# Kernel optimization log

Hardware: AMD Instinct MI355X
Metric: run time of the kernel (lower is better)

The kernel has to match this reference:

```python
import jax, jax.numpy as jnp
import numpy as np

B, T, C = 2, 2048, 1024
H = 4 * C           # MLP hidden (4*n_embd)
E_DYN = 7           # num_experts - static_experts
TOP_K = 2           # num_experts_per_tok
MOE_LOSS_COEF = 0.01


def setup_inputs() -> dict:
    key = jax.random.key(0)
    ks = jax.random.split(key, 6)
    s = 0.02
    x = jax.random.normal(ks[0], (B, T, C), dtype=jnp.float32)
    gate_w = jax.random.normal(ks[1], (C, E_DYN), dtype=jnp.float32) * s
    w1 = jax.random.normal(ks[2], (E_DYN, C, H), dtype=jnp.float32) * s   # dynamic experts c_fc
    w2 = jax.random.normal(ks[3], (E_DYN, H, C), dtype=jnp.float32) * s   # dynamic experts c_proj
    w1s = jax.random.normal(ks[4], (C, H), dtype=jnp.float32) * s         # static expert c_fc
    w2s = jax.random.normal(ks[5], (H, C), dtype=jnp.float32) * s         # static expert c_proj
    return {"x": x, "gate_w": gate_w, "w1": w1, "w2": w2, "w1s": w1s, "w2s": w2s}


def reference(x, gate_w, w1, w2, w1s, w2s):
    b, t, c = x.shape
    xf = x.reshape(-1, c)                                   # [N, C]
    n = xf.shape[0]

    # static expert (always applied)
    y_static = jax.nn.gelu(xf @ w1s, approximate=False) @ w2s  # [N, C]

    # gating: top-k + softmax over selected scores
    scores = xf @ gate_w                                    # [N, E]
    topk_scores, topk_idx = jax.lax.top_k(scores, TOP_K)    # [N, K]
    topk_w = jax.nn.softmax(topk_scores, axis=-1)           # [N, K]

    # dense dispatch weights [N, E] (top_k indices are distinct -> set is safe)
    probs = jnp.zeros((n, E_DYN), dtype=x.dtype)
    probs = probs.at[jnp.arange(n)[:, None], topk_idx].set(topk_w)

    # all-expert MLP then weighted combine (same math as masked per-expert dispatch)
    h = jax.nn.gelu(jnp.einsum('nc,ech->enh', xf, w1), approximate=False)  # [E, N, H]
    y_all = jnp.einsum('enh,ehc->enc', h, w2)               # [E, N, C]
    y_dyn = jnp.einsum('ne,enc->nc', probs, y_all)          # [N, C]

    y = (y_dyn + y_static).reshape(b, t, c)

    # variance_penalty auxiliary loss
    expert_usage = probs.mean(axis=0)                       # [E]
    variance = jnp.mean((expert_usage - expert_usage.mean()) ** 2)
    aux = MOE_LOSS_COEF * variance
    return y, aux
```

## Files before the change

### kernel.cpp

```cpp
#include <hip/hip_runtime.h>
#include <hip/hip_bf16.h>
#include <math.h>

#define N_TOK 4096
#define C_DIM 1024
#define H_DIM 4096
#define NEXP 7
#define NGRP 8
#define HCAP 13184

typedef __attribute__((ext_vector_type(8))) short short8;
typedef __attribute__((ext_vector_type(4))) float floatx4;

static const size_t OFF_COUNTS = 0;
static const size_t OFF_CURSOR = 64;
static const size_t OFF_BASE   = 128;
static const size_t OFF_PCOUNT = 192;
static const size_t OFF_CNT8   = 256;
static const size_t OFF_USAGE  = 320;
static const size_t OFF_TOPKI  = 4096;
static const size_t OFF_TOPKW  = OFF_TOPKI + 8192ull * 4;
static const size_t OFF_ETOK   = OFF_TOPKW + 8192ull * 4;
static const size_t OFF_EWT    = OFF_ETOK + (size_t)HCAP * 4;
static const size_t OFF_EIDX   = OFF_EWT + (size_t)HCAP * 4;
static const size_t OFF_XB     = 262144;
static const size_t OFF_W1T    = OFF_XB + (size_t)N_TOK * C_DIM * 2;
static const size_t OFF_W2T    = OFF_W1T + (size_t)NGRP * H_DIM * C_DIM * 2;
static const size_t OFF_H      = OFF_W2T + (size_t)NGRP * C_DIM * H_DIM * 2;

static __device__ __forceinline__ unsigned short f2bf(float f) {
    __hip_bfloat16 b = __float2bfloat16(f);
    return *reinterpret_cast<unsigned short*>(&b);
}
static __device__ __forceinline__ float bf2f(unsigned short u) {
    unsigned int v = ((unsigned int)u) << 16;
    return __builtin_bit_cast(float, v);
}

static __device__ __forceinline__ float gelu_f(float v) {
    float z = v * 0.70710678118654752f;
    float az = fabsf(z);
    float t = 1.0f / (1.0f + 0.3275911f * az);
    float poly = t * (0.254829592f + t * (-0.284496736f + t * (1.421413741f +
                 t * (-1.453152027f + t * 1.061405429f))));
    float erf_abs = 1.0f - poly * __expf(-az * az);
    float erf_v = (z < 0.f) ? -erf_abs : erf_abs;
    return 0.5f * v * (1.0f + erf_v);
}

static __device__ __forceinline__ void gll16(const void* g, void* l) {
    __builtin_amdgcn_global_load_lds((const __attribute__((address_space(1))) void*)g,
                                     (__attribute__((address_space(3))) void*)l, 16, 0, 0);
}

__global__ void init_small_kernel(int* counts, int* cursor, float* usage) {
    int i = threadIdx.x;
    if (i < 8) { counts[i] = 0; cursor[i] = 0; usage[i] = 0.f; }
}

__global__ void convert_x_kernel(const float* __restrict__ x, unsigned short* __restrict__ xb) {
    int i = blockIdx.x * 256 + threadIdx.x;
    float4 v = ((const float4*)x)[i];
    ushort4 o;
    o.x = f2bf(v.x); o.y = f2bf(v.y); o.z = f2bf(v.z); o.w = f2bf(v.w);
    ((ushort4*)xb)[i] = o;
}

__global__ __launch_bounds__(256) void transpose_cvt_kernel(
    const float* __restrict__ dyn, const float* __restrict__ stat,
    __hip_bfloat16* __restrict__ dst, int R, int S)
{
    int e = blockIdx.z;
    const float* src = (e < NEXP) ? (dyn + (size_t)e * R * S) : stat;
    __hip_bfloat16* d = dst + (size_t)e * R * S;
    int s0 = blockIdx.x * 32, r0 = blockIdx.y * 64;
    int tx = threadIdx.x & 31, ty = threadIdx.x >> 5;
    __shared__ float t[64][33];
#pragma unroll
    for (int i = 0; i < 8; i++) {
        int r = ty + i * 8;
        t[r][tx] = src[(size_t)(r0 + r) * S + s0 + tx];
    }
    __syncthreads();
    int tx2 = threadIdx.x & 63, ty2 = threadIdx.x >> 6;
#pragma unroll
    for (int i = 0; i < 8; i++) {
        int s = ty2 + i * 4;
        d[(size_t)(s0 + s) * R + r0 + tx2] = __float2bfloat16(t[tx2][s]);
    }
}

__global__ __launch_bounds__(256) void gate_kernel(
    const float* __restrict__ x, const float* __restrict__ gw,
    int* __restrict__ topki, float* __restrict__ topkw,
    int* counts, float* usage)
{
    int wid = threadIdx.x >> 6, lane = threadIdx.x & 63;
    int t = blockIdx.x * 4 + wid;
    float s[NEXP];
#pragma unroll
    for (int e = 0; e < NEXP; e++) s[e] = 0.f;
    for (int c = lane; c < C_DIM; c += 64) {
        float xv = x[(size_t)t * C_DIM + c];
#pragma unroll
        for (int e = 0; e < NEXP; e++) s[e] += xv * gw[c * NEXP + e];
    }
#pragma unroll
    for (int e = 0; e < NEXP; e++)
        for (int off = 32; off > 0; off >>= 1) s[e] += __shfl_xor(s[e], off);
    if (lane == 0) {
        int e0 = 0;
        for (int e = 1; e < NEXP; e++) if (s[e] > s[e0]) e0 = e;
        int e1 = -1;
        for (int e = 0; e < NEXP; e++) {
            if (e == e0) continue;
            if (e1 < 0 || s[e] > s[e1]) e1 = e;
        }
        float w0 = 1.f / (1.f + expf(s[e1] - s[e0]));
        float w1 = 1.f - w0;
        topki[t * 2] = e0; topki[t * 2 + 1] = e1;
        topkw[t * 2] = w0; topkw[t * 2 + 1] = w1;
        atomicAdd(&counts[e0], 1); atomicAdd(&counts[e1], 1);
        atomicAdd(&usage[e0], w0); atomicAdd(&usage[e1], w1);
    }
}

__global__ __launch_bounds__(256) void prefix_kernel(
    const int* counts, const float* usage,
    int* base, int* pcount, int* cnt8,
    int* etok, float* ewt, float* y, int aux_index)
{
    __shared__ int sb[NGRP], sc[NGRP], sp[NGRP];
    if (threadIdx.x == 0) {
        int run = 0;
        for (int g = 0; g < NEXP; g++) {
            int c = counts[g];
            int p = (c + 127) & ~127;
            base[g] = run; pcount[g] = p; cnt8[g] = c;
            sb[g] = run; sc[g] = c; sp[g] = p;
            run += p;
        }
        base[NEXP] = run; pcount[NEXP] = N_TOK; cnt8[NEXP] = N_TOK;
        sb[NEXP] = run; sc[NEXP] = N_TOK; sp[NEXP] = N_TOK;
        float u[NEXP]; float mean = 0.f;
        for (int e = 0; e < NEXP; e++) { u[e] = usage[e] / (float)N_TOK; mean += u[e]; }
        mean /= (float)NEXP;
        float var = 0.f;
        for (int e = 0; e < NEXP; e++) { float d = u[e] - mean; var += d * d; }
        var /= (float)NEXP;
        y[aux_index] = 0.01f * var;
    }
    __syncthreads();
    for (int i = threadIdx.x; i < N_TOK; i += 256) {
        etok[sb[NEXP] + i] = i; ewt[sb[NEXP] + i] = 1.0f;
    }
    for (int g = 0; g < NEXP; g++) {
        for (int i = sc[g] + (int)threadIdx.x; i < sp[g]; i += 256) {
            etok[sb[g] + i] = 0; ewt[sb[g] + i] = 0.f;
        }
    }
}

__global__ void scatter_kernel(const int* __restrict__ topki, const float* __restrict__ topkw,
                               const int* __restrict__ base, int* cursor,
                               int* __restrict__ etok, float* __restrict__ ewt,
                               int* __restrict__ eidx)
{
    int i = blockIdx.x * 256 + threadIdx.x;
    int t = i >> 1;
    int e = topki[i];
    float w = topkw[i];
    int pos = atomicAdd(&cursor[e], 1);
    int idx = base[e] + pos;
    etok[idx] = t; ewt[idx] = w;
    eidx[i] = idx;
}

__global__ __launch_bounds__(256) void gemm1_kernel(
    const __hip_bfloat16* __restrict__ xb,
    const __hip_bfloat16* __restrict__ w1t,
    __hip_bfloat16* __restrict__ h,
    const int* __restrict__ etok,
    const int* __restrict__ base,
    const int* __restrict__ pcount)
{
    int g = blockIdx.z, mt = blockIdx.y, ct = blockIdx.x;
    if (mt * 128 >= pcount[g]) return;
    int eb = base[g];

    __shared__ __align__(16) char AlsB[2 * 8192];
    __shared__ __align__(16) char BlsB[2 * 8192];

    int tid = threadIdx.x;
    int lane = tid & 63, wid = tid >> 6;
    int quad = lane >> 4, l16 = lane & 15;
    int wm = wid >> 1, wn = wid & 1;
    int rsub = lane >> 2, chunk = lane & 3;

    const char* gA[2]; const char* gB[2];
    char* lA[2]; char* lB[2];
#pragma unroll
    for (int j = 0; j < 2; j++) {
        int rowA = wid * 32 + j * 16 + rsub;
        int tok = etok[eb + mt * 128 + rowA];
        gA[j] = (const char*)(xb + (size_t)tok * C_DIM) + chunk * 16;
        lA[j] = AlsB + (wid * 32 + j * 16) * 64;
        int rowB = wid * 32 + j * 16 + rsub;
        gB[j] = (const char*)(w1t + ((size_t)g * H_DIM + ct * 128 + rowB) * C_DIM) + chunk * 16;
        lB[j] = BlsB + (wid * 32 + j * 16) * 64;
    }

    floatx4 acc[4][4] = {};
    for (int k0 = 0; k0 < C_DIM; k0 += 64) {
        size_t koff = (size_t)k0 * 2;
#pragma unroll
        for (int s = 0; s < 2; s++) {
            size_t so = koff + (size_t)s * 64;
            gll16(gA[0] + so, lA[0] + s * 8192);
            gll16(gA[1] + so, lA[1] + s * 8192);
            gll16(gB[0] + so, lB[0] + s * 8192);
            gll16(gB[1] + so, lB[1] + s * 8192);
        }
        __syncthreads();
#pragma unroll
        for (int s = 0; s < 2; s++) {
            short8 a[4], b[4];
#pragma unroll
            for (int i = 0; i < 4; i++) {
                a[i] = *(const short8*)(AlsB + s * 8192 + (((wm * 64 + i * 16 + l16) * 32 + quad * 8) * 2));
                b[i] = *(const short8*)(BlsB + s * 8192 + (((wn * 64 + i * 16 + l16) * 32 + quad * 8) * 2));
            }
#pragma unroll
            for (int i = 0; i < 4; i++)
#pragma unroll
                for (int j = 0; j < 4; j++)
                    acc[i][j] = __builtin_amdgcn_mfma_f32_16x16x32_bf16(a[i], b[j], acc[i][j], 0, 0, 0);
        }
        __syncthreads();
    }

#pragma unroll
    for (int i = 0; i < 4; i++) {
        int rbase = mt * 128 + wm * 64 + i * 16 + quad * 4;
#pragma unroll
        for (int reg = 0; reg < 4; reg++) {
            size_t hrow = (size_t)(eb + rbase + reg) * H_DIM;
#pragma unroll
            for (int j = 0; j < 4; j++) {
                int cc = ct * 128 + wn * 64 + j * 16 + l16;
                h[hrow + cc] = __float2bfloat16(gelu_f(acc[i][j][reg]));
            }
        }
    }
}

__global__ __launch_bounds__(256) void gemm2_kernel(
    const __hip_bfloat16* __restrict__ h,
    const __hip_bfloat16* __restrict__ w2t,
    unsigned short* __restrict__ yp,
    const int* __restrict__ base,
    const int* __restrict__ pcount)
{
    int g = blockIdx.z, ct = blockIdx.x, mt = blockIdx.y;
    if (mt * 128 >= pcount[g]) return;
    int eb = base[g];

    __shared__ __align__(16) char AlsB[2 * 8192];
    __shared__ __align__(16) char BlsB[2 * 8192];

    int tid = threadIdx.x;
    int lane = tid & 63, wid = tid >> 6;
    int quad = lane >> 4, l16 = lane & 15;
    int wm = wid >> 1, wn = wid & 1;
    int rsub = lane >> 2, chunk = lane & 3;

    const char* gA[2]; const char* gB[2];
    char* lA[2]; char* lB[2];
#pragma unroll
    for (int j = 0; j < 2; j++) {
        int rowA = wid * 32 + j * 16 + rsub;
        gA[j] = (const char*)(h + (size_t)(eb + mt * 128 + rowA) * H_DIM) + chunk * 16;
        lA[j] = AlsB + (wid * 32 + j * 16) * 64;
        int rowB = wid * 32 + j * 16 + rsub;
        gB[j] = (const char*)(w2t + ((size_t)g * C_DIM + ct * 128 + rowB) * H_DIM) + chunk * 16;
        lB[j] = BlsB + (wid * 32 + j * 16) * 64;
    }

    floatx4 acc[4][4] = {};
    for (int k0 = 0; k0 < H_DIM; k0 += 64) {
        size_t koff = (size_t)k0 * 2;
#pragma unroll
        for (int s = 0; s < 2; s++) {
            size_t so = koff + (size_t)s * 64;
            gll16(gA[0] + so, lA[0] + s * 8192);
            gll16(gA[1] + so, lA[1] + s * 8192);
            gll16(gB[0] + so, lB[0] + s * 8192);
            gll16(gB[1] + so, lB[1] + s * 8192);
        }
        __syncthreads();
#pragma unroll
        for (int s = 0; s < 2; s++) {
            short8 a[4], b[4];
#pragma unroll
            for (int i = 0; i < 4; i++) {
                a[i] = *(const short8*)(AlsB + s * 8192 + (((wm * 64 + i * 16 + l16) * 32 + quad * 8) * 2));
                b[i] = *(const short8*)(BlsB + s * 8192 + (((wn * 64 + i * 16 + l16) * 32 + quad * 8) * 2));
            }
#pragma unroll
            for (int i = 0; i < 4; i++)
#pragma unroll
                for (int j = 0; j < 4; j++)
                    acc[i][j] = __builtin_amdgcn_mfma_f32_16x16x32_bf16(a[i], b[j], acc[i][j], 0, 0, 0);
        }
        __syncthreads();
    }

#pragma unroll
    for (int i = 0; i < 4; i++) {
        int rl0 = mt * 128 + wm * 64 + i * 16 + quad * 4;
#pragma unroll
        for (int reg = 0; reg < 4; reg++) {
            size_t yrow = (size_t)(eb + rl0 + reg) * C_DIM;
#pragma unroll
            for (int j = 0; j < 4; j++) {
                int cc = ct * 128 + wn * 64 + j * 16 + l16;
                yp[yrow + cc] = f2bf(acc[i][j][reg]);
            }
        }
    }
}

__global__ __launch_bounds__(256) void combine_kernel(
    const unsigned short* __restrict__ yp,
    const int* __restrict__ eidx,
    const float* __restrict__ topkw,
    const int* __restrict__ base,
    float* __restrict__ y)
{
    int t = blockIdx.x;
    int i0 = eidx[t * 2], i1 = eidx[t * 2 + 1];
    float w0 = topkw[t * 2], w1 = topkw[t * 2 + 1];
    int is = base[NEXP] + t;
    int c = threadIdx.x * 4;
    ushort4 a = *(const ushort4*)(yp + (size_t)i0 * C_DIM + c);
    ushort4 b = *(const ushort4*)(yp + (size_t)i1 * C_DIM + c);
    ushort4 s = *(const ushort4*)(yp + (size_t)is * C_DIM + c);
    float4 o;
    o.x = w0 * bf2f(a.x) + w1 * bf2f(b.x) + bf2f(s.x);
    o.y = w0 * bf2f(a.y) + w1 * bf2f(b.y) + bf2f(s.y);
    o.z = w0 * bf2f(a.z) + w1 * bf2f(b.z) + bf2f(s.z);
    o.w = w0 * bf2f(a.w) + w1 * bf2f(b.w) + bf2f(s.w);
    *(float4*)(y + (size_t)t * C_DIM + c) = o;
}

extern "C" void kernel_launch(void* const* d_in, const int* in_sizes, int n_in,
                              void* d_out, int out_size, void* d_ws, size_t ws_size,
                              hipStream_t stream) {
    const float* x      = (const float*)d_in[0];
    const float* gate_w = (const float*)d_in[1];
    const float* w1     = (const float*)d_in[2];
    const float* w2     = (const float*)d_in[3];
    const float* w1s    = (const float*)d_in[4];
    const float* w2s    = (const float*)d_in[5];
    float* y = (float*)d_out;
    char* ws = (char*)d_ws;

    int*   counts = (int*)(ws + OFF_COUNTS);
    int*   cursor = (int*)(ws + OFF_CURSOR);
    int*   base   = (int*)(ws + OFF_BASE);
    int*   pcount = (int*)(ws + OFF_PCOUNT);
    int*   cnt8   = (int*)(ws + OFF_CNT8);
    float* usage  = (float*)(ws + OFF_USAGE);
    int*   topki  = (int*)(ws + OFF_TOPKI);
    float* topkw  = (float*)(ws + OFF_TOPKW);
    int*   etok   = (int*)(ws + OFF_ETOK);
    float* ewt    = (float*)(ws + OFF_EWT);
    int*   eidx   = (int*)(ws + OFF_EIDX);
    unsigned short* xb_u = (unsigned short*)(ws + OFF_XB);
    __hip_bfloat16* xb  = (__hip_bfloat16*)(ws + OFF_XB);
    __hip_bfloat16* w1t = (__hip_bfloat16*)(ws + OFF_W1T);
    __hip_bfloat16* w2t = (__hip_bfloat16*)(ws + OFF_W2T);
    __hip_bfloat16* hbuf = (__hip_bfloat16*)(ws + OFF_H);
    unsigned short* yp  = (unsigned short*)(ws + OFF_W1T);

    init_small_kernel<<<1, 64, 0, stream>>>(counts, cursor, usage);

    convert_x_kernel<<<(N_TOK * C_DIM / 4) / 256, 256, 0, stream>>>(x, xb_u);
    transpose_cvt_kernel<<<dim3(H_DIM / 32, C_DIM / 64, NGRP), 256, 0, stream>>>(w1, w1s, w1t, C_DIM, H_DIM);
    transpose_cvt_kernel<<<dim3(C_DIM / 32, H_DIM / 64, NGRP), 256, 0, stream>>>(w2, w2s, w2t, H_DIM, C_DIM);

    gate_kernel<<<N_TOK / 4, 256, 0, stream>>>(x, gate_w, topki, topkw, counts, usage);
    prefix_kernel<<<1, 256, 0, stream>>>(counts, usage, base, pcount, cnt8, etok, ewt, y, N_TOK * C_DIM);
    scatter_kernel<<<(N_TOK * 2) / 256, 256, 0, stream>>>(topki, topkw, base, cursor, etok, ewt, eidx);

    gemm1_kernel<<<dim3(H_DIM / 128, 64, NGRP), 256, 0, stream>>>(xb, w1t, hbuf, etok, base, pcount);
    gemm2_kernel<<<dim3(C_DIM / 128, 64, NGRP), 256, 0, stream>>>(hbuf, w2t, yp, base, pcount);
    combine_kernel<<<N_TOK, 256, 0, stream>>>(yp, eidx, topkw, base, y);
}
```

Baseline: 814.6 us.

## Triple-buffer GEMM K-loop with async loads, LDS swizzle, XCD-aware gemm2 tiling

Both expert GEMMs drop the two-sync-per-64K loop for a three-stage ring of 32-wide K tiles. Global-to-LDS loads are issued two stages ahead and waited on with explicit vmcnt and barrier calls, and the MFMA block is wrapped in setprio. LDS rows use an XOR chunk swizzle to cut bank conflicts. gemm2 moves to a 1D grid that keeps blocks sharing an mt tile on the same XCD for L2 reuse, and the weight transpose kernel now uses paired float2/ushort2 accesses. The hand-placed waitcnt and barrier sequence is fragile, and the third buffer adds LDS use, which may lower occupancy.

New measurement: 843.6 us. 1.04x slower.

```diff
diff --git a/kernel.cpp b/kernel.cpp
--- a/kernel.cpp
+++ b/kernel.cpp
@@ -53,6 +53,39 @@
                                      (__attribute__((address_space(3))) void*)l, 16, 0, 0);
 }
 
+template <int VM> static __device__ __forceinline__ void wait_vm() {
+    if constexpr (VM == 8) asm volatile("s_waitcnt vmcnt(8)" ::: "memory");
+    else if constexpr (VM == 4) asm volatile("s_waitcnt vmcnt(4)" ::: "memory");
+    else asm volatile("s_waitcnt vmcnt(0)" ::: "memory");
+}
+static __device__ __forceinline__ void barf() {
+    __builtin_amdgcn_s_barrier();
+    asm volatile("" ::: "memory");
+}
+static __device__ __forceinline__ void lgkm0_bar() {
+    asm volatile("s_waitcnt lgkmcnt(0)" ::: "memory");
+    __builtin_amdgcn_s_barrier();
+    asm volatile("" ::: "memory");
+}
+
+static __device__ __forceinline__ void mfma_step(const char* Ap, const char* Bp,
+    int wm, int wn, int l16, int rswz, floatx4 (&acc)[4][4])
+{
+    short8 a[4], b[4];
+#pragma unroll
+    for (int i = 0; i < 4; i++) {
+        a[i] = *(const short8*)(Ap + ((wm * 64 + i * 16 + l16) * 64 + rswz));
+        b[i] = *(const short8*)(Bp + ((wn * 64 + i * 16 + l16) * 64 + rswz));
+    }
+    __builtin_amdgcn_s_setprio(1);
+#pragma unroll
+    for (int i = 0; i < 4; i++)
+#pragma unroll
+        for (int j = 0; j < 4; j++)
+            acc[i][j] = __builtin_amdgcn_mfma_f32_16x16x32_bf16(a[i], b[j], acc[i][j], 0, 0, 0);
+    __builtin_amdgcn_s_setprio(0);
+}
+
 __global__ void init_small_kernel(int* counts, int* cursor, float* usage) {
     int i = threadIdx.x;
     if (i < 8) { counts[i] = 0; cursor[i] = 0; usage[i] = 0.f; }
@@ -72,21 +105,25 @@
 {
     int e = blockIdx.z;
     const float* src = (e < NEXP) ? (dyn + (size_t)e * R * S) : stat;
-    __hip_bfloat16* d = dst + (size_t)e * R * S;
+    unsigned short* d = (unsigned short*)(dst + (size_t)e * R * S);
     int s0 = blockIdx.x * 32, r0 = blockIdx.y * 64;
-    int tx = threadIdx.x & 31, ty = threadIdx.x >> 5;
     __shared__ float t[64][33];
-#pragma unroll
-    for (int i = 0; i < 8; i++) {
-        int r = ty + i * 8;
-        t[r][tx] = src[(size_t)(r0 + r) * S + s0 + tx];
+    int tx4 = threadIdx.x & 15, ty4 = threadIdx.x >> 4;
+#pragma unroll
+    for (int i = 0; i < 4; i++) {
+        int r = ty4 + i * 16;
+        float2 v = *(const float2*)(src + (size_t)(r0 + r) * S + s0 + tx4 * 2);
+        t[r][tx4 * 2] = v.x; t[r][tx4 * 2 + 1] = v.y;
     }
     __syncthreads();
-    int tx2 = threadIdx.x & 63, ty2 = threadIdx.x >> 6;
-#pragma unroll
-    for (int i = 0; i < 8; i++) {
-        int s = ty2 + i * 4;
-        d[(size_t)(s0 + s) * R + r0 + tx2] = __float2bfloat16(t[tx2][s]);
+    int tx3 = threadIdx.x & 31, ty3 = threadIdx.x >> 5;
+#pragma unroll
+    for (int i = 0; i < 4; i++) {
+        int s = ty3 + i * 8;
+        int r = tx3 * 2;
+        ushort2 o;
+        o.x = f2bf(t[r][s]); o.y = f2bf(t[r + 1][s]);
+        *(ushort2*)(d + (size_t)(s0 + s) * R + r0 + r) = o;
     }
 }
 
@@ -146,7 +183,7 @@
         for (int e = 0; e < NEXP; e++) { u[e] = usage[e] / (float)N_TOK; mean += u[e]; }
         mean /= (float)NEXP;
         float var = 0.f;
-        for (int e = 0; e < NEXP; e++) { float d = u[e] - mean; var += d * d; }
+        for (int e = 0; e < NEXP; e++) { float dd = u[e] - mean; var += dd * dd; }
         var /= (float)NEXP;
         y[aux_index] = 0.01f * var;
     }
@@ -188,56 +225,52 @@
     if (mt * 128 >= pcount[g]) return;
     int eb = base[g];
 
-    __shared__ __align__(16) char AlsB[2 * 8192];
-    __shared__ __align__(16) char BlsB[2 * 8192];
+    __shared__ __align__(16) char Ab[3][8192];
+    __shared__ __align__(16) char Bb[3][8192];
 
     int tid = threadIdx.x;
     int lane = tid & 63, wid = tid >> 6;
     int quad = lane >> 4, l16 = lane & 15;
     int wm = wid >> 1, wn = wid & 1;
     int rsub = lane >> 2, chunk = lane & 3;
-
-    const char* gA[2]; const char* gB[2];
-    char* lA[2]; char* lB[2];
+    int swzc = chunk ^ ((rsub >> 1) & 3);
+    int rswz = (quad ^ ((l16 >> 1) & 3)) * 16;
+
+    const char* gA[2]; const char* gB[2]; int lo[2];
 #pragma unroll
     for (int j = 0; j < 2; j++) {
-        int rowA = wid * 32 + j * 16 + rsub;
-        int tok = etok[eb + mt * 128 + rowA];
-        gA[j] = (const char*)(xb + (size_t)tok * C_DIM) + chunk * 16;
-        lA[j] = AlsB + (wid * 32 + j * 16) * 64;
-        int rowB = wid * 32 + j * 16 + rsub;
-        gB[j] = (const char*)(w1t + ((size_t)g * H_DIM + ct * 128 + rowB) * C_DIM) + chunk * 16;
-        lB[j] = BlsB + (wid * 32 + j * 16) * 64;
-    }
+        int row = wid * 32 + j * 16 + rsub;
+        int tok = etok[eb + mt * 128 + row];
+        gA[j] = (const char*)(xb + (size_t)tok * C_DIM) + swzc * 16;
+        gB[j] = (const char*)(w1t + ((size_t)g * H_DIM + ct * 128 + row) * C_DIM) + swzc * 16;
+        lo[j] = (wid * 32 + j * 16) * 64;
+    }
+
+#define STG(p, kt) do { size_t so = (size_t)(kt) * 64; \
+        gll16(gA[0] + so, Ab[p] + lo[0]); \
+        gll16(gA[1] + so, Ab[p] + lo[1]); \
+        gll16(gB[0] + so, Bb[p] + lo[0]); \
+        gll16(gB[1] + so, Bb[p] + lo[1]); } while (0)
 
     floatx4 acc[4][4] = {};
-    for (int k0 = 0; k0 < C_DIM; k0 += 64) {
-        size_t koff = (size_t)k0 * 2;
-#pragma unroll
-        for (int s = 0; s < 2; s++) {
-            size_t so = koff + (size_t)s * 64;
-            gll16(gA[0] + so, lA[0] + s * 8192);
-            gll16(gA[1] + so, lA[1] + s * 8192);
-            gll16(gB[0] + so, lB[0] + s * 8192);
-            gll16(gB[1] + so, lB[1] + s * 8192);
-        }
-        __syncthreads();
-#pragma unroll
-        for (int s = 0; s < 2; s++) {
-            short8 a[4], b[4];
-#pragma unroll
-            for (int i = 0; i < 4; i++) {
-                a[i] = *(const short8*)(AlsB + s * 8192 + (((wm * 64 + i * 16 + l16) * 32 + quad * 8) * 2));
-                b[i] = *(const short8*)(BlsB + s * 8192 + (((wn * 64 + i * 16 + l16) * 32 + quad * 8) * 2));
-            }
-#pragma unroll
-            for (int i = 0; i < 4; i++)
-#pragma unroll
-                for (int j = 0; j < 4; j++)
-                    acc[i][j] = __builtin_amdgcn_mfma_f32_16x16x32_bf16(a[i], b[j], acc[i][j], 0, 0, 0);
-        }
-        __syncthreads();
-    }
+    const int nt = C_DIM / 32;
+    STG(0, 0); STG(1, 1);
+    int p = 0;
+    for (int t = 0; t + 2 < nt; ++t) {
+        int pn = p + 2; if (pn >= 3) pn -= 3;
+        STG(pn, t + 2);
+        wait_vm<8>();
+        barf();
+        mfma_step(Ab[p], Bb[p], wm, wn, l16, rswz, acc);
+        lgkm0_bar();
+        if (++p == 3) p = 0;
+    }
+    wait_vm<4>(); barf();
+    mfma_step(Ab[0], Bb[0], wm, wn, l16, rswz, acc);
+    lgkm0_bar();
+    wait_vm<0>(); barf();
+    mfma_step(Ab[1], Bb[1], wm, wn, l16, rswz, acc);
+#undef STG
 
 #pragma unroll
     for (int i = 0; i < 4; i++) {
@@ -261,59 +294,60 @@
     const int* __restrict__ base,
     const int* __restrict__ pcount)
 {
-    int g = blockIdx.z, ct = blockIdx.x, mt = blockIdx.y;
+    int id = blockIdx.x;
+    int xcd = id & 7;
+    int jj  = id >> 3;
+    int ct  = jj & 7;
+    int g4  = xcd + ((jj >> 3) << 3);
+    int mt  = g4 & 63, g = g4 >> 6;
     if (mt * 128 >= pcount[g]) return;
     int eb = base[g];
 
-    __shared__ __align__(16) char AlsB[2 * 8192];
-    __shared__ __align__(16) char BlsB[2 * 8192];
+    __shared__ __align__(16) char Ab[3][8192];
+    __shared__ __align__(16) char Bb[3][8192];
 
     int tid = threadIdx.x;
     int lane = tid & 63, wid = tid >> 6;
     int quad = lane >> 4, l16 = lane & 15;
     int wm = wid >> 1, wn = wid & 1;
     int rsub = lane >> 2, chunk = lane & 3;
-
-    const char* gA[2]; const char* gB[2];
-    char* lA[2]; char* lB[2];
+    int swzc = chunk ^ ((rsub >> 1) & 3);
+    int rswz = (quad ^ ((l16 >> 1) & 3)) * 16;
+
+    const char* gA[2]; const char* gB[2]; int lo[2];
 #pragma unroll
     for (int j = 0; j < 2; j++) {
-        int rowA = wid * 32 + j * 16 + rsub;
-        gA[j] = (const char*)(h + (size_t)(eb + mt * 128 + rowA) * H_DIM) + chunk * 16;
-        lA[j] = AlsB + (wid * 32 + j * 16) * 64;
-        int rowB = wid * 32 + j * 16 + rsub;
-        gB[j] = (const char*)(w2t + ((size_t)g * C_DIM + ct * 128 + rowB) * H_DIM) + chunk * 16;
-        lB[j] = BlsB + (wid * 32 + j * 16) * 64;
-    }
+        int row = wid * 32 + j * 16 + rsub;
+        gA[j] = (const char*)(h + (size_t)(eb + mt * 128 + row) * H_DIM) + swzc * 16;
+        gB[j] = (const char*)(w2t + ((size_t)g * C_DIM + ct * 128 + row) * H_DIM) + swzc * 16;
+        lo[j] = (wid * 32 + j * 16) * 64;
+    }
+
+#define STG(p, kt) do { size_t so = (size_t)(kt) * 64; \
+        gll16(gA[0] + so, Ab[p] + lo[0]); \
+        gll16(gA[1] + so, Ab[p] + lo[1]); \
+        gll16(gB[0] + so, Bb[p] + lo[0]); \
+        gll16(gB[1] + so, Bb[p] + lo[1]); } while (0)
 
     floatx4 acc[4][4] = {};
-    for (int k0 = 0; k0 < H_DIM; k0 += 64) {
-        size_t koff = (size_t)k0 * 2;
-#pragma unroll
-        for (int s = 0; s < 2; s++) {
-            size_t so = koff + (size_t)s * 64;
-            gll16(gA[0] + so, lA[0] + s * 8192);
-            gll16(gA[1] + so, lA[1] + s * 8192);
-            gll16(gB[0] + so, lB[0] + s * 8192);
-            gll16(gB[1] + so, lB[1] + s * 8192);
-        }
-        __syncthreads();
-#pragma unroll
-        for (int s = 0; s < 2; s++) {
-            short8 a[4], b[4];
-#pragma unroll
-            for (int i = 0; i < 4; i++) {
-                a[i] = *(const short8*)(AlsB + s * 8192 + (((wm * 64 + i * 16 + l16) * 32 + quad * 8) * 2));
-                b[i] = *(const short8*)(BlsB + s * 8192 + (((wn * 64 + i * 16 + l16) * 32 + quad * 8) * 2));
-            }
-#pragma unroll
-            for (int i = 0; i < 4; i++)
-#pragma unroll
-                for (int j = 0; j < 4; j++)
-                    acc[i][j] = __builtin_amdgcn_mfma_f32_16x16x32_bf16(a[i], b[j], acc[i][j], 0, 0, 0);
-        }
-        __syncthreads();
-    }
+    const int nt = H_DIM / 32;
+    STG(0, 0); STG(1, 1);
+    int p = 0;
+    for (int t = 0; t + 2 < nt; ++t) {
+        int pn = p + 2; if (pn >= 3) pn -= 3;
+        STG(pn, t + 2);
+        wait_vm<8>();
+        barf();
+        mfma_step(Ab[p], Bb[p], wm, wn, l16, rswz, acc);
+        lgkm0_bar();
+        if (++p == 3) p = 0;
+    }
+    wait_vm<4>(); barf();
+    mfma_step(Ab[0], Bb[0], wm, wn, l16, rswz, acc);
+    lgkm0_bar();
+    wait_vm<0>(); barf();
+    mfma_step(Ab[1], Bb[1], wm, wn, l16, rswz, acc);
+#undef STG
 
 #pragma unroll
     for (int i = 0; i < 4; i++) {
@@ -394,6 +428,6 @@
     scatter_kernel<<<(N_TOK * 2) / 256, 256, 0, stream>>>(topki, topkw, base, cursor, etok, ewt, eidx);
 
     gemm1_kernel<<<dim3(H_DIM / 128, 64, NGRP), 256, 0, stream>>>(xb, w1t, hbuf, etok, base, pcount);
-    gemm2_kernel<<<dim3(C_DIM / 128, 64, NGRP), 256, 0, stream>>>(hbuf, w2t, yp, base, pcount);
+    gemm2_kernel<<<4096, 256, 0, stream>>>(hbuf, w2t, yp, base, pcount);
     combine_kernel<<<N_TOK, 256, 0, stream>>>(yp, eidx, topkw, base, y);
 }
```
